# Kernel optimization log

Hardware: AMD Instinct MI355X
Metric: run time of the kernel (lower is better)

The kernel has to match this reference:

```python
import jax, jax.numpy as jnp
import numpy as np

B, INP, OUP, FGROUP, H, W = 32, 256, 256, 8, 64, 64
CG = INP // FGROUP  # channels per group in GLGF fc1 layers


def conv3x3(x, w):
    # x: (N,1,H,W), w: (1,1,3,3); stride 1, padding 1 (SAME)
    return jax.lax.conv_general_dilated(
        x, w, window_strides=(1, 1), padding='SAME',
        dimension_numbers=('NCHW', 'OIHW', 'NCHW'))


def setup_inputs() -> dict:
    key = jax.random.key(0)
    ks = jax.random.split(key, 8)
    return {
        'x': jax.random.normal(ks[0], (B, INP, H, W), dtype=jnp.float32),
        # GLGF params (all 1x1 convs, bias=False), stored as dense matrices
        'w1l': jax.random.normal(ks[1], (FGROUP, CG, CG), dtype=jnp.float32) * 0.05,   # wn_fc1_l (groups=fgroup)
        'w1g1': jax.random.normal(ks[2], (FGROUP, CG), dtype=jnp.float32) * 0.05,      # wn_fc1_g1 (inp->fgroup, groups=fgroup)
        'w1g2': jax.random.normal(ks[3], (INP, FGROUP), dtype=jnp.float32) * 0.05,     # wn_fc1_g2 (fgroup->inp dense)
        'w2l': jax.random.normal(ks[4], (INP, OUP), dtype=jnp.float32) * 0.05,         # wn_fc2_l (groups=inp): input ch i -> oup outputs
        'w2g': jax.random.normal(ks[5], (INP,), dtype=jnp.float32) * 0.05,             # wn_fc2_g (inp->1 dense)
        'conv1_w': jax.random.normal(ks[6], (1, 1, 3, 3), dtype=jnp.float32) * 0.1,
        'conv2_w': jax.random.normal(ks[7], (1, 1, 3, 3), dtype=jnp.float32) * 0.1,
    }


def reference(x, w1l, w1g1, w1g2, w2l, w2g, conv1_w, conv2_w):
    b, c, h, w_ = x.shape
    fgroup, cg, _ = w1l.shape
    oup = w2l.shape[1]

    # adaptive_avg_pool2d(x, (1,1)) -> (B, inp) descriptor
    g = x.mean(axis=(2, 3))                                   # (B, inp)
    gg = g.reshape(b, fgroup, cg)

    # GLGF: fc1_l (grouped) + fc1_g2(fc1_g1) (squeeze to fgroup then expand)
    local = jnp.einsum('bgi,goi->bgo', gg, w1l).reshape(b, c)  # (B, inp)
    glob = jnp.einsum('bgi,gi->bg', gg, w1g1) @ w1g2.T         # (B, inp)
    s = jax.nn.sigmoid(local + glob)                           # (B, inp)

    # fc2_l (groups=inp): torch channel order is (input_ch g, out j) -> g*oup + j
    # fc2_g adds a per-sample scalar to every channel
    xw = s[:, :, None] * w2l + (s @ w2g)[:, None, None]        # (B, inp, oup)
    # WA_1Conv reinterprets the flat (oup*inp) channels as (oup, inp)
    Wdyn = xw.reshape(b, oup, c)                               # (B, oup, inp)

    # grouped conv with groups=batch, ksize=1 == per-sample matmul
    y = jnp.einsum('bihw,boi->bohw', x, Wdyn)                  # (B, oup, H, W)

    # channel gating: mean over channels -> conv3x3 -> sigmoid -> conv3x3
    cmap = y.mean(axis=1, keepdims=True)                       # (B, 1, H, W)
    cmap = conv3x3(cmap, conv1_w)
    cmap = jax.nn.sigmoid(cmap)
    cmap = conv3x3(cmap, conv2_w)
    return y * cmap
```

## Files before the change

### kernel.cpp

```cpp
#include <hip/hip_runtime.h>
#include <hip/hip_bf16.h>

typedef float  f32x4  __attribute__((ext_vector_type(4)));
typedef short  bf16x8 __attribute__((ext_vector_type(8)));

__device__ __forceinline__ short f2bf(float f) {
    union { __hip_bfloat16 h; short s; } u;
    u.h = __float2bfloat16(f);
    return u.s;
}

__device__ __forceinline__ void gload_lds16(const void* g, void* l) {
    __builtin_amdgcn_global_load_lds(
        (const __attribute__((address_space(1))) unsigned int*)g,
        (__attribute__((address_space(3))) unsigned int*)l, 16, 0, 0);
}

__device__ __forceinline__ void nt_load8(const float* p, float* dst) {
    const f32x4* vp = reinterpret_cast<const f32x4*>(p);
    f32x4 a = __builtin_nontemporal_load(vp);
    f32x4 b = __builtin_nontemporal_load(vp + 1);
    *reinterpret_cast<f32x4*>(dst)     = a;
    *reinterpret_cast<f32x4*>(dst + 4) = b;
}

__global__ __launch_bounds__(256) void transpose_kernel(const float* __restrict__ x,
                                                        short* __restrict__ xt,
                                                        float* __restrict__ gpart,
                                                        float* __restrict__ xsump) {
    const int pchunk = blockIdx.x;
    const int cchunk = blockIdx.y;
    const int c0 = cchunk * 64;
    const int b  = blockIdx.z;
    const int tid = threadIdx.x;
    const int cpair = tid >> 3;
    const int poct  = tid & 7;
    const int p0 = pchunk * 64;

    __shared__ unsigned int tile[64 * 32];
    __shared__ float xred[4 * 64];

    const float* rowA = x + ((size_t)(b * 256 + c0 + 2 * cpair)) * 4096 + p0 + poct * 8;
    const float* rowB = rowA + 4096;
    float av[8], bv[8];
    nt_load8(rowA, av);
    nt_load8(rowB, bv);

    float sA = 0.f, sB = 0.f;
    #pragma unroll
    for (int e = 0; e < 8; ++e) { sA += av[e]; sB += bv[e]; }
    sA += __shfl_xor(sA, 1, 64); sA += __shfl_xor(sA, 2, 64); sA += __shfl_xor(sA, 4, 64);
    sB += __shfl_xor(sB, 1, 64); sB += __shfl_xor(sB, 2, 64); sB += __shfl_xor(sB, 4, 64);
    if (poct == 0) {
        gpart[((size_t)(b * 256 + c0 + 2 * cpair)) * 64 + pchunk] = sA;
        gpart[((size_t)(b * 256 + c0 + 2 * cpair + 1)) * 64 + pchunk] = sB;
    }

    float xs[8];
    #pragma unroll
    for (int e = 0; e < 8; ++e) {
        float v = av[e] + bv[e];
        v += __shfl_xor(v, 8, 64);
        v += __shfl_xor(v, 16, 64);
        v += __shfl_xor(v, 32, 64);
        xs[e] = v;
    }
    if ((tid & 56) == 0) {
        int wv = tid >> 6;
        #pragma unroll
        for (int e = 0; e < 8; ++e) xred[wv * 64 + poct * 8 + e] = xs[e];
    }

    const int s = cpair >> 2, w = cpair & 3;
    #pragma unroll
    for (int e = 0; e < 8; ++e) {
        int p = poct * 8 + e;
        unsigned int u = (unsigned int)(unsigned short)f2bf(av[e]) |
                         ((unsigned int)(unsigned short)f2bf(bv[e]) << 16);
        tile[p * 32 + ((s ^ poct) << 2) + w] = u;
    }
    __syncthreads();

    if (tid < 64) {
        float v = xred[tid] + xred[64 + tid] + xred[128 + tid] + xred[192 + tid];
        xsump[((size_t)(cchunk * 32 + b)) * 4096 + p0 + tid] = v;
    }

    const int so = tid & 7;
    #pragma unroll
    for (int h = 0; h < 2; ++h) {
        int p = (tid >> 3) + h * 32;
        int sp = so ^ ((p >> 3) & 7);
        uint4 v = *reinterpret_cast<const uint4*>(&tile[p * 32 + sp * 4]);
        *reinterpret_cast<uint4*>(xt + ((size_t)b * 4096 + p0 + p) * 256 + c0 + so * 8) = v;
    }
}

__global__ __launch_bounds__(256) void prep_cmap0_kernel(
    const short* __restrict__ xt, const float* __restrict__ gpart,
    const float* __restrict__ w1l, const float* __restrict__ w1g1,
    const float* __restrict__ w1g2, const float* __restrict__ w2l,
    const float* __restrict__ w2g, const float* __restrict__ xsump,
    float* __restrict__ s_out, short* __restrict__ w2l_bf,
    float* __restrict__ cmap0, float* __restrict__ txs) {
    const int b = blockIdx.y;
    const int tid = threadIdx.x;
    if (b >= 32) {
        int seg = blockIdx.x;
        const float* src = w2l + seg * 4096;
        short* dst = w2l_bf + seg * 4096;
        #pragma unroll
        for (int it = 0; it < 4; ++it) {
            float4 v = *reinterpret_cast<const float4*>(src + it * 1024 + tid * 4);
            short4 o;
            o.x = f2bf(v.x); o.y = f2bf(v.y); o.z = f2bf(v.z); o.w = f2bf(v.w);
            *reinterpret_cast<short4*>(dst + it * 1024 + tid * 4) = o;
        }
        return;
    }
    __shared__ float gs[256];
    __shared__ float zs[8];
    __shared__ float ss[256];
    __shared__ float red[4];
    __shared__ float vs[256];
    {
        const float4* gp = reinterpret_cast<const float4*>(gpart + (size_t)(b * 256 + tid) * 64);
        float acc = 0.f;
        #pragma unroll
        for (int j = 0; j < 16; ++j) { float4 v = gp[j]; acc += v.x + v.y + v.z + v.w; }
        gs[tid] = acc * (1.0f / 4096.0f);
    }
    __syncthreads();
    if (tid < 8) {
        float z = 0.f;
        for (int i = 0; i < 32; ++i) z += gs[tid * 32 + i] * w1g1[tid * 32 + i];
        zs[tid] = z;
    }
    __syncthreads();
    {
        int grp = tid >> 5, o = tid & 31;
        float local = 0.f;
        #pragma unroll 4
        for (int i = 0; i < 32; ++i) local += gs[grp * 32 + i] * w1l[grp * 1024 + o * 32 + i];
        float glob = 0.f;
        #pragma unroll
        for (int gg = 0; gg < 8; ++gg) glob += zs[gg] * w1g2[tid * 8 + gg];
        float sv = 1.0f / (1.0f + expf(-(local + glob)));
        ss[tid] = sv;
        if (blockIdx.x == 0) s_out[b * 256 + tid] = sv;
        float tv = sv * w2g[tid];
        #pragma unroll
        for (int off = 32; off; off >>= 1) tv += __shfl_down(tv, off, 64);
        if ((tid & 63) == 0) red[tid >> 6] = tv;
    }
    __syncthreads();
    const float tb = red[0] + red[1] + red[2] + red[3];
    {
        float v = 0.f;
        for (int o2 = 0; o2 < 256; ++o2) v += ss[o2] * w2l[o2 * 256 + tid];
        vs[tid] = v * (1.0f / 256.0f);
    }
    __syncthreads();

    const int p = blockIdx.x * 256 + tid;
    const uint4* row = reinterpret_cast<const uint4*>(xt + ((size_t)b * 4096 + p) * 256);
    float acc = 0.f;
    #pragma unroll 8
    for (int it = 0; it < 32; ++it) {
        uint4 u = row[it];
        const unsigned int* uw = reinterpret_cast<const unsigned int*>(&u);
        #pragma unroll
        for (int j = 0; j < 4; ++j) {
            unsigned int wrd = uw[j];
            union { unsigned int u; float f; } lo, hi;
            lo.u = wrd << 16;
            hi.u = wrd & 0xffff0000u;
            acc += lo.f * vs[it * 8 + 2 * j] + hi.f * vs[it * 8 + 2 * j + 1];
        }
    }
    float xsv = 0.f;
    #pragma unroll
    for (int part = 0; part < 4; ++part)
        xsv += xsump[((size_t)(part * 32 + b)) * 4096 + p];
    float tx = tb * xsv;
    cmap0[b * 4096 + p] = acc + tx;
    txs[b * 4096 + p] = tx;
}

__global__ __launch_bounds__(512) void gemm_epi_kernel(
    const short* __restrict__ xt, const short* __restrict__ w2l_bf,
    const float* __restrict__ s, const float* __restrict__ txs,
    const float* __restrict__ cmap0, const float* __restrict__ w9a,
    const float* __restrict__ w9b, float* __restrict__ out) {
    const int b  = blockIdx.z;
    const int r  = blockIdx.x;
    const int p0 = r * 64;
    const int tid  = threadIdx.x;
    const int lane = tid & 63;
    const int w    = tid >> 6;
    const int wm = w >> 1, wn = w & 1;

    __shared__ short Alds[2][256 * 64];
    __shared__ short Xlds[2][64 * 64];

    const int sl   = (lane & 7) ^ (lane >> 3);
    const int lrow = lane >> 3;

    float wa[9], wb[9];
    #pragma unroll
    for (int i = 0; i < 9; ++i) { wa[i] = w9a[i]; wb[i] = w9b[i]; }
    float c0v = 0.f;
    if (tid < 320) {
        int i5 = tid >> 6, cc = tid & 63;
        int rr = r - 2 + i5;
        if (rr >= 0 && rr < 64) c0v = cmap0[(size_t)b * 4096 + rr * 64 + cc];
    }
    float txr[2], sv[4][4];
    #pragma unroll
    for (int n = 0; n < 2; ++n) {
        int p = p0 + wn * 32 + n * 16 + (lane & 15);
        txr[n] = txs[b * 4096 + p];
    }
    #pragma unroll
    for (int m = 0; m < 4; ++m)
        #pragma unroll
        for (int q = 0; q < 4; ++q)
            sv[m][q] = s[b * 256 + wm * 64 + m * 16 + (lane >> 4) * 4 + q];

    f32x4 acc[4][2] = {};

    auto STAGE = [&](int bi, int ks) {
        #pragma unroll
        for (int j = 0; j < 4; ++j) {
            int chunk = w * 4 + j;
            int row = chunk * 8 + lrow;
            gload_lds16(w2l_bf + (size_t)row * 256 + ks + sl * 8,
                        (char*)(&Alds[bi][0]) + chunk * 1024);
        }
        int prow = w * 8 + lrow;
        gload_lds16(xt + ((size_t)b * 4096 + p0 + prow) * 256 + ks + sl * 8,
                    (char*)(&Xlds[bi][0]) + w * 1024);
    };

    STAGE(0, 0);
    #pragma unroll
    for (int t = 0; t < 4; ++t) {
        const int bi = t & 1;
        if (t < 3) {
            STAGE(bi ^ 1, (t + 1) * 64);
            asm volatile("s_waitcnt vmcnt(5)" ::: "memory");
        } else {
            asm volatile("s_waitcnt vmcnt(0)" ::: "memory");
        }
        __builtin_amdgcn_s_barrier();
        asm volatile("" ::: "memory");
        #pragma unroll
        for (int kk = 0; kk < 2; ++kk) {
            bf16x8 af[4], bfr[2];
            const int ss = kk * 4 + (lane >> 4);
            #pragma unroll
            for (int m = 0; m < 4; ++m) {
                int o = wm * 64 + m * 16 + (lane & 15);
                af[m] = *reinterpret_cast<const bf16x8*>(
                    (char*)(&Alds[bi][0]) + o * 128 + ((ss ^ (lane & 7)) * 16));
            }
            #pragma unroll
            for (int n = 0; n < 2; ++n) {
                int p = wn * 32 + n * 16 + (lane & 15);
                bfr[n] = *reinterpret_cast<const bf16x8*>(
                    (char*)(&Xlds[bi][0]) + p * 128 + ((ss ^ (lane & 7)) * 16));
            }
            #pragma unroll
            for (int m = 0; m < 4; ++m)
                #pragma unroll
                for (int n = 0; n < 2; ++n)
                    acc[m][n] = __builtin_amdgcn_mfma_f32_16x16x32_bf16(af[m], bfr[n], acc[m][n], 0, 0, 0);
        }
        asm volatile("" ::: "memory");
        __builtin_amdgcn_s_barrier();
    }

    __syncthreads();
    float* csc  = (float*)&Alds[0][0];
    float* midl = csc + 320;
    float* cmsl = midl + 192;
    if (tid < 320) csc[tid] = c0v;
    __syncthreads();
    if (tid < 192) {
        int i3 = tid >> 6, cc = tid & 63;
        int rm = r - 1 + i3;
        float a = 0.f;
        if (rm >= 0 && rm < 64) {
            #pragma unroll
            for (int dy = 0; dy < 3; ++dy)
                #pragma unroll
                for (int dx = -1; dx <= 1; ++dx) {
                    int c2 = cc + dx;
                    if (c2 >= 0 && c2 < 64)
                        a += csc[(i3 + dy) * 64 + c2] * wa[dy * 3 + dx + 1];
                }
            a = 1.0f / (1.0f + expf(-a));
        }
        midl[tid] = a;
    }
    __syncthreads();
    if (tid < 64) {
        float a = 0.f;
        #pragma unroll
        for (int i3 = 0; i3 < 3; ++i3)
            #pragma unroll
            for (int dx = -1; dx <= 1; ++dx) {
                int c2 = tid + dx;
                if (c2 >= 0 && c2 < 64)
                    a += midl[i3 * 64 + c2] * wb[i3 * 3 + dx + 1];
            }
        cmsl[tid] = a;
    }
    __syncthreads();

    #pragma unroll
    for (int n = 0; n < 2; ++n) {
        int pc = wn * 32 + n * 16 + (lane & 15);
        int p = p0 + pc;
        float cm = cmsl[pc];
        #pragma unroll
        for (int m = 0; m < 4; ++m) {
            #pragma unroll
            for (int q = 0; q < 4; ++q) {
                int o = wm * 64 + m * 16 + (lane >> 4) * 4 + q;
                float yv = (sv[m][q] * acc[m][n][q] + txr[n]) * cm;
                __builtin_nontemporal_store(yv, &out[((size_t)b * 256 + o) * 4096 + p]);
            }
        }
    }
}

extern "C" void kernel_launch(void* const* d_in, const int* in_sizes, int n_in,
                              void* d_out, int out_size, void* d_ws, size_t ws_size,
                              hipStream_t stream) {
    const float* x       = (const float*)d_in[0];
    const float* w1l     = (const float*)d_in[1];
    const float* w1g1    = (const float*)d_in[2];
    const float* w1g2    = (const float*)d_in[3];
    const float* w2l     = (const float*)d_in[4];
    const float* w2g     = (const float*)d_in[5];
    const float* conv1_w = (const float*)d_in[6];
    const float* conv2_w = (const float*)d_in[7];
    float* out = (float*)d_out;

    float* wsf    = (float*)d_ws;
    float* s      = wsf;
    float* cmap0  = wsf + 8192;
    float* txs    = wsf + 139264;
    float* gpart  = wsf + 270336;
    float* xsump  = wsf + 794624;
    short* w2l_bf = (short*)(wsf + 1318912);
    short* xt     = (short*)(wsf + 1351680);

    transpose_kernel<<<dim3(64, 4, 32), 256, 0, stream>>>(x, xt, gpart, xsump);
    prep_cmap0_kernel<<<dim3(16, 33), 256, 0, stream>>>(
        xt, gpart, w1l, w1g1, w1g2, w2l, w2g, xsump, s, w2l_bf, cmap0, txs);
    gemm_epi_kernel<<<dim3(64, 1, 32), 512, 0, stream>>>(
        xt, w2l_bf, s, txs, cmap0, conv1_w, conv2_w, out);
}
```

Measured before the change: 118.7 us.

## Shrink GEMM-epilogue block to 256 threads with K=32 stages for higher occupancy

The fused GEMM+epilogue kernel drops from 512 to 256 threads per block, with each wave computing twice as many output rows (8x2 MFMA tiles). The K loop is halved to 32-wide stages over 8 iterations, which halves the LDS footprint and uses a new XOR swizzle for 64-byte rows. Epilogue operands (s, txs, cmap0, conv weights) are now loaded late instead of held in registers across the GEMM. The intent is to fit more blocks per CU and reduce register pressure. The cost is more barriers per block, and the larger per-wave accumulator could increase VGPR use.

```diff
diff --git a/kernel.cpp b/kernel.cpp
--- a/kernel.cpp
+++ b/kernel.cpp
@@ -187,7 +187,7 @@
     txs[b * 4096 + p] = tx;
 }
 
-__global__ __launch_bounds__(512) void gemm_epi_kernel(
+__global__ __launch_bounds__(256, 4) void gemm_epi_kernel(
     const short* __restrict__ xt, const short* __restrict__ w2l_bf,
     const float* __restrict__ s, const float* __restrict__ txs,
     const float* __restrict__ cmap0, const float* __restrict__ w9a,
@@ -200,91 +200,82 @@
     const int w    = tid >> 6;
     const int wm = w >> 1, wn = w & 1;
 
-    __shared__ short Alds[2][256 * 64];
-    __shared__ short Xlds[2][64 * 64];
-
-    const int sl   = (lane & 7) ^ (lane >> 3);
-    const int lrow = lane >> 3;
-
-    float wa[9], wb[9];
-    #pragma unroll
-    for (int i = 0; i < 9; ++i) { wa[i] = w9a[i]; wb[i] = w9b[i]; }
-    float c0v = 0.f;
-    if (tid < 320) {
-        int i5 = tid >> 6, cc = tid & 63;
-        int rr = r - 2 + i5;
-        if (rr >= 0 && rr < 64) c0v = cmap0[(size_t)b * 4096 + rr * 64 + cc];
-    }
-    float txr[2], sv[4][4];
-    #pragma unroll
-    for (int n = 0; n < 2; ++n) {
-        int p = p0 + wn * 32 + n * 16 + (lane & 15);
-        txr[n] = txs[b * 4096 + p];
-    }
-    #pragma unroll
-    for (int m = 0; m < 4; ++m)
-        #pragma unroll
-        for (int q = 0; q < 4; ++q)
-            sv[m][q] = s[b * 256 + wm * 64 + m * 16 + (lane >> 4) * 4 + q];
-
-    f32x4 acc[4][2] = {};
+    __shared__ short Alds[2][256 * 32];
+    __shared__ short Xlds[2][64 * 32];
+
+    const int l2 = lane >> 2;
+
+    f32x4 acc[8][2] = {};
 
     auto STAGE = [&](int bi, int ks) {
         #pragma unroll
         for (int j = 0; j < 4; ++j) {
-            int chunk = w * 4 + j;
-            int row = chunk * 8 + lrow;
-            gload_lds16(w2l_bf + (size_t)row * 256 + ks + sl * 8,
-                        (char*)(&Alds[bi][0]) + chunk * 1024);
-        }
-        int prow = w * 8 + lrow;
-        gload_lds16(xt + ((size_t)b * 4096 + p0 + prow) * 256 + ks + sl * 8,
-                    (char*)(&Xlds[bi][0]) + w * 1024);
+            int row = j * 64 + w * 16 + l2;
+            int sig = (lane & 3) ^ ((row ^ (row >> 2)) & 3);
+            gload_lds16(w2l_bf + (size_t)row * 256 + ks + sig * 8,
+                        (char*)(&Alds[bi][0]) + j * 4096 + w * 1024);
+        }
+        {
+            int prow = w * 16 + l2;
+            int sig = (lane & 3) ^ ((prow ^ (prow >> 2)) & 3);
+            gload_lds16(xt + ((size_t)b * 4096 + p0 + prow) * 256 + ks + sig * 8,
+                        (char*)(&Xlds[bi][0]) + w * 1024);
+        }
     };
 
     STAGE(0, 0);
     #pragma unroll
-    for (int t = 0; t < 4; ++t) {
+    for (int t = 0; t < 8; ++t) {
         const int bi = t & 1;
-        if (t < 3) {
-            STAGE(bi ^ 1, (t + 1) * 64);
+        if (t < 7) {
+            STAGE(bi ^ 1, (t + 1) * 32);
             asm volatile("s_waitcnt vmcnt(5)" ::: "memory");
         } else {
             asm volatile("s_waitcnt vmcnt(0)" ::: "memory");
         }
         __builtin_amdgcn_s_barrier();
         asm volatile("" ::: "memory");
-        #pragma unroll
-        for (int kk = 0; kk < 2; ++kk) {
-            bf16x8 af[4], bfr[2];
-            const int ss = kk * 4 + (lane >> 4);
-            #pragma unroll
-            for (int m = 0; m < 4; ++m) {
-                int o = wm * 64 + m * 16 + (lane & 15);
-                af[m] = *reinterpret_cast<const bf16x8*>(
-                    (char*)(&Alds[bi][0]) + o * 128 + ((ss ^ (lane & 7)) * 16));
+        bf16x8 bfr[2];
+        #pragma unroll
+        for (int n = 0; n < 2; ++n) {
+            int p = wn * 32 + n * 16 + (lane & 15);
+            int sl = (lane >> 4) ^ ((p ^ (p >> 2)) & 3);
+            bfr[n] = *reinterpret_cast<const bf16x8*>(
+                (char*)(&Xlds[bi][0]) + p * 64 + sl * 16);
+        }
+        #pragma unroll
+        for (int mh = 0; mh < 2; ++mh) {
+            bf16x8 af[4];
+            #pragma unroll
+            for (int i = 0; i < 4; ++i) {
+                int o = wm * 128 + (mh * 4 + i) * 16 + (lane & 15);
+                int sl = (lane >> 4) ^ ((o ^ (o >> 2)) & 3);
+                af[i] = *reinterpret_cast<const bf16x8*>(
+                    (char*)(&Alds[bi][0]) + o * 64 + sl * 16);
             }
             #pragma unroll
-            for (int n = 0; n < 2; ++n) {
-                int p = wn * 32 + n * 16 + (lane & 15);
-                bfr[n] = *reinterpret_cast<const bf16x8*>(
-                    (char*)(&Xlds[bi][0]) + p * 128 + ((ss ^ (lane & 7)) * 16));
-            }
-            #pragma unroll
-            for (int m = 0; m < 4; ++m)
+            for (int i = 0; i < 4; ++i)
                 #pragma unroll
                 for (int n = 0; n < 2; ++n)
-                    acc[m][n] = __builtin_amdgcn_mfma_f32_16x16x32_bf16(af[m], bfr[n], acc[m][n], 0, 0, 0);
+                    acc[mh * 4 + i][n] = __builtin_amdgcn_mfma_f32_16x16x32_bf16(
+                        af[i], bfr[n], acc[mh * 4 + i][n], 0, 0, 0);
         }
         asm volatile("" ::: "memory");
         __builtin_amdgcn_s_barrier();
     }
 
+    float wa[9], wb[9];
+    #pragma unroll
+    for (int i = 0; i < 9; ++i) { wa[i] = w9a[i]; wb[i] = w9b[i]; }
     __syncthreads();
     float* csc  = (float*)&Alds[0][0];
     float* midl = csc + 320;
     float* cmsl = midl + 192;
-    if (tid < 320) csc[tid] = c0v;
+    for (int idx = tid; idx < 320; idx += 256) {
+        int i5 = idx >> 6, cc = idx & 63;
+        int rr = r - 2 + i5;
+        csc[idx] = (rr >= 0 && rr < 64) ? cmap0[(size_t)b * 4096 + rr * 64 + cc] : 0.f;
+    }
     __syncthreads();
     if (tid < 192) {
         int i3 = tid >> 6, cc = tid & 63;
@@ -323,12 +314,14 @@
         int pc = wn * 32 + n * 16 + (lane & 15);
         int p = p0 + pc;
         float cm = cmsl[pc];
-        #pragma unroll
-        for (int m = 0; m < 4; ++m) {
+        float tx = txs[b * 4096 + p];
+        #pragma unroll
+        for (int m = 0; m < 8; ++m) {
             #pragma unroll
             for (int q = 0; q < 4; ++q) {
-                int o = wm * 64 + m * 16 + (lane >> 4) * 4 + q;
-                float yv = (sv[m][q] * acc[m][n][q] + txr[n]) * cm;
+                int o = wm * 128 + m * 16 + (lane >> 4) * 4 + q;
+                float sv = s[b * 256 + o];
+                float yv = (sv * acc[m][n][q] + tx) * cm;
                 __builtin_nontemporal_store(yv, &out[((size_t)b * 256 + o) * 4096 + p]);
             }
         }
@@ -360,6 +353,6 @@
     transpose_kernel<<<dim3(64, 4, 32), 256, 0, stream>>>(x, xt, gpart, xsump);
     prep_cmap0_kernel<<<dim3(16, 33), 256, 0, stream>>>(
         xt, gpart, w1l, w1g1, w1g2, w2l, w2g, xsump, s, w2l_bf, cmap0, txs);
-    gemm_epi_kernel<<<dim3(64, 1, 32), 512, 0, stream>>>(
+    gemm_epi_kernel<<<dim3(64, 1, 32), 256, 0, stream>>>(
         xt, w2l_bf, s, txs, cmap0, conv1_w, conv2_w, out);
 }
```

Measured after the change: 129.5 us. +9.1%, slower.
